# Optimization experiments

Measured on AMD Instinct MI355X. Metric: run time of the kernel, lower is better.

## Reference

```python
import jax, jax.numpy as jnp
import numpy as np

N = 33554432
NUM_CLASSES = 1000


def setup_inputs() -> dict:
    key = jax.random.key(0)
    k1, k2, k3 = jax.random.split(key, 3)
    confidences = jax.random.uniform(k1, (N,), dtype=jnp.float32)  # max-prob in [0,1)
    predictions = jax.random.randint(k2, (N,), 0, NUM_CLASSES, dtype=jnp.int64)
    labels = jax.random.randint(k3, (N,), 0, NUM_CLASSES, dtype=jnp.int64)
    return {"confidences": confidences, "predictions": predictions,
            "labels": labels, "n_bins": 10}


def reference(confidences, predictions, labels, n_bins):
    # Bin i covers (i/n_bins, (i+1)/n_bins]; conf == 0.0 goes to bin 0 (matches torch loop).
    n = confidences.shape[0]
    boundaries = jnp.linspace(0.0, 1.0, n_bins + 1, dtype=confidences.dtype)
    # searchsorted over upper boundaries: first upper >= conf -> bin index
    bins = jnp.searchsorted(boundaries[1:], confidences, side="left")
    bins = jnp.clip(bins, 0, n_bins - 1)

    acc = (predictions == labels).astype(confidences.dtype)
    ones = jnp.ones_like(confidences)

    cnt = jax.ops.segment_sum(ones, bins, num_segments=n_bins)
    acc_sum = jax.ops.segment_sum(acc, bins, num_segments=n_bins)
    conf_sum = jax.ops.segment_sum(confidences, bins, num_segments=n_bins)

    nonempty = cnt > 0
    safe_cnt = jnp.where(nonempty, cnt, jnp.ones_like(cnt))
    gap = jnp.abs(conf_sum / safe_cnt - acc_sum / safe_cnt)
    prop = cnt / n
    ece = jnp.sum(jnp.where(nonempty, gap * prop, jnp.zeros_like(gap)))
    return ece
```

## Files before the change

### kernel.cpp

```cpp
#include <hip/hip_runtime.h>


#define NBLK 2048
#define TPB  256
#define MAXB 256


__global__ __launch_bounds__(TPB) void ece_partial(
    const float* __restrict__ conf, const int* __restrict__ pred,
    const int* __restrict__ lab, const int* __restrict__ nbins_p,
    int n, int cap,
    unsigned* __restrict__ ws_cnt, unsigned* __restrict__ ws_acc,
    float* __restrict__ ws_conf)
{
  const int nb = nbins_p[0];
  const int tid = blockIdx.x * blockDim.x + threadIdx.x;
  const int nthreads = gridDim.x * blockDim.x;

  __shared__ unsigned s_ca[TPB / 64][10];
  __shared__ float    s_cs[TPB / 64][10];
  __shared__ unsigned g_cnt[MAXB];
  __shared__ unsigned g_acc[MAXB];
  __shared__ float    g_conf[MAXB];

  if (nb == 10 && cap >= 10) {
    unsigned ca[10];
    float    cs[10];
#pragma unroll
    for (int j = 0; j < 10; ++j) { ca[j] = 0u; cs[j] = 0.0f; }

    const int n4 = n >> 2;
    const float4* c4 = (const float4*)conf;
    const int4*   p4 = (const int4*)pred;
    const int4*   l4 = (const int4*)lab;

    for (int i = tid; i < n4; i += nthreads) {
      float4 c = c4[i];
      int4   p = p4[i];
      int4   l = l4[i];
      float cc[4] = {c.x, c.y, c.z, c.w};
      int   ok[4] = {p.x == l.x, p.y == l.y, p.z == l.z, p.w == l.w};
#pragma unroll
      for (int e = 0; e < 4; ++e) {
        float v = cc[e];
        int bin = 0;
#pragma unroll
        for (int j = 1; j <= 10; ++j) bin += ((float)j * 0.1f < v) ? 1 : 0;
        if (bin > 9) bin = 9;
#pragma unroll
        for (int j = 0; j < 10; ++j) {
          bool m = (bin == j);
          ca[j] += m ? (0x10000u | (unsigned)ok[e]) : 0u;
          cs[j] += m ? v : 0.0f;
        }
      }
    }
    for (int i = (n4 << 2) + tid; i < n; i += nthreads) {
      float v = conf[i];
      int okk = (pred[i] == lab[i]);
      int bin = 0;
#pragma unroll
      for (int j = 1; j <= 10; ++j) bin += ((float)j * 0.1f < v) ? 1 : 0;
      if (bin > 9) bin = 9;
#pragma unroll
      for (int j = 0; j < 10; ++j) {
        bool m = (bin == j);
        ca[j] += m ? (0x10000u | (unsigned)okk) : 0u;
        cs[j] += m ? v : 0.0f;
      }
    }

    const int lane = threadIdx.x & 63;
    const int wv   = threadIdx.x >> 6;
#pragma unroll
    for (int j = 0; j < 10; ++j) {
      unsigned a = ca[j];
      float    s = cs[j];
#pragma unroll
      for (int d = 32; d > 0; d >>= 1) {
        a += __shfl_xor(a, d, 64);
        s += __shfl_xor(s, d, 64);
      }
      if (lane == 0) { s_ca[wv][j] = a; s_cs[wv][j] = s; }
    }
    __syncthreads();
    if (threadIdx.x < 10) {
      unsigned tot = 0; float tc = 0.0f;
#pragma unroll
      for (int w = 0; w < TPB / 64; ++w) { tot += s_ca[w][threadIdx.x]; tc += s_cs[w][threadIdx.x]; }
      const int o = threadIdx.x * gridDim.x + blockIdx.x;
      ws_cnt[o]  = tot >> 16;
      ws_acc[o]  = tot & 0xFFFFu;
      ws_conf[o] = tc;
    }
  } else {
    int nbc = nb < 1 ? 1 : nb;
    if (nbc > MAXB) nbc = MAXB;
    if (nbc > cap) nbc = (cap < 1) ? 1 : cap;
    for (int j = threadIdx.x; j < nbc; j += blockDim.x) { g_cnt[j] = 0u; g_acc[j] = 0u; g_conf[j] = 0.0f; }
    __syncthreads();
    const float delta = 1.0f / (float)nb;
    for (int i = tid; i < n; i += nthreads) {
      float v = conf[i];
      int okk = (pred[i] == lab[i]);
      int bin = (int)(v * (float)nb);
      if (bin > nb - 1) bin = nb - 1;
      if (bin < 0) bin = 0;
      while (bin < nb - 1 && (float)(bin + 1) * delta < v) ++bin;
      while (bin > 0 && !((float)bin * delta < v)) --bin;
      if (bin > nbc - 1) bin = nbc - 1;
      atomicAdd(&g_cnt[bin], 1u);
      atomicAdd(&g_acc[bin], (unsigned)okk);
      atomicAdd(&g_conf[bin], v);
    }
    __syncthreads();
    for (int j = threadIdx.x; j < nbc; j += blockDim.x) {
      ws_cnt[j * gridDim.x + blockIdx.x]  = g_cnt[j];
      ws_acc[j * gridDim.x + blockIdx.x]  = g_acc[j];
      ws_conf[j * gridDim.x + blockIdx.x] = g_conf[j];
    }
  }
}

__global__ __launch_bounds__(640) void ece_final(
    const unsigned* __restrict__ ws_cnt, const unsigned* __restrict__ ws_acc,
    const float* __restrict__ ws_conf, const int* __restrict__ nbins_p,
    int n, int cap, float* __restrict__ out)
{
  int nb = nbins_p[0];
  if (nb < 1) nb = 1;
  int mx = cap < MAXB ? cap : MAXB;
  if (nb > mx) nb = mx;
  const int wv   = threadIdx.x >> 6;
  const int lane = threadIdx.x & 63;
  __shared__ double terms[MAXB];
  for (int j = threadIdx.x; j < MAXB; j += blockDim.x) terms[j] = 0.0;
  __syncthreads();
  for (int bin = wv; bin < nb; bin += 10) {
    unsigned long long cnt = 0, acc = 0;
    double cs = 0.0;
    for (int b = lane; b < NBLK; b += 64) {
      cnt += ws_cnt[bin * NBLK + b];
      acc += ws_acc[bin * NBLK + b];
      cs  += (double)ws_conf[bin * NBLK + b];
    }
#pragma unroll
    for (int d = 32; d > 0; d >>= 1) {
      cnt += __shfl_xor(cnt, d, 64);
      acc += __shfl_xor(acc, d, 64);
      cs  += __shfl_xor(cs, d, 64);
    }
    if (lane == 0) {
      double t = 0.0;
      if (cnt > 0) {
        double dc = (double)cnt;
        t = fabs(cs / dc - (double)acc / dc) * (dc / (double)n);
      }
      terms[bin] = t;
    }
  }
  __syncthreads();
  if (threadIdx.x == 0) {
    double e = 0.0;
    for (int j = 0; j < nb; ++j) e += terms[j];
    out[0] = (float)e;
  }
}

extern "C" void kernel_launch(void* const* d_in, const int* in_sizes, int n_in,
                              void* d_out, int out_size, void* d_ws, size_t ws_size,
                              hipStream_t stream) {
  const float* conf = (const float*)d_in[0];
  const int*   pred = (const int*)d_in[1];
  const int*   lab  = (const int*)d_in[2];
  const int*   nbp  = (const int*)d_in[3];
  const int n = in_sizes[0];

  size_t per = ws_size / 3;
  int cap = (int)(per / ((size_t)NBLK * sizeof(unsigned)));
  if (cap > MAXB) cap = MAXB;
  unsigned* ws_cnt = (unsigned*)d_ws;
  unsigned* ws_acc = (unsigned*)((char*)d_ws + (size_t)cap * NBLK * sizeof(unsigned));
  float*    ws_conf = (float*)((char*)d_ws + 2ull * (size_t)cap * NBLK * sizeof(unsigned));

  ece_partial<<<NBLK, TPB, 0, stream>>>(conf, pred, lab, nbp, n, cap, ws_cnt, ws_acc, ws_conf);
  ece_final<<<1, 640, 0, stream>>>(ws_cnt, ws_acc, ws_conf, nbp, n, cap, (float*)d_out);
}
```

Measured before the change: 387.6 us.

## Use cumulative threshold sums with wave ballot counts instead of per-bin masks

Replaces per-element one-hot binning with cumulative per-threshold accumulators (count of v > j*0.1), counting via wave ballot+popcount and recovering per-bin values by differencing in the final kernel. This removes the bin index computation and the 10-way select chain, leaving 9 compare/select pairs per element. The main loop uses a fixed iteration count, and the final kernel reads with float4 loads. Partial results become floats, and sums of floats over thresholds are differenced, which can add rounding error.

```diff
diff --git a/kernel.cpp b/kernel.cpp
--- a/kernel.cpp
+++ b/kernel.cpp
@@ -3,95 +3,115 @@
 
 #define NBLK 2048
 #define TPB  256
+#define NTH  (NBLK * TPB)
 #define MAXB 256
 
+#define SB(J)                                                   \
+  { bool g = ((float)(J) * 0.1f) < v;                           \
+    c##J += (unsigned)__popcll(__ballot(g));                    \
+    a##J += g ? okf : 0.0f;                                     \
+    t##J += g ? v : 0.0f; }
+
+#define SLOT(cx, px, lx)                                        \
+  { float v = (cx);                                             \
+    float okf = ((px) == (lx)) ? 1.0f : 0.0f;                   \
+    cAll += (unsigned)__popcll(__ballot(1));                    \
+    tAll += v; aAll += okf;                                     \
+    SB(1) SB(2) SB(3) SB(4) SB(5) SB(6) SB(7) SB(8) SB(9) }
+
+#define WRED(x)                                                 \
+  { x += __shfl_xor(x, 32, 64); x += __shfl_xor(x, 16, 64);     \
+    x += __shfl_xor(x, 8, 64);  x += __shfl_xor(x, 4, 64);      \
+    x += __shfl_xor(x, 2, 64);  x += __shfl_xor(x, 1, 64); }
 
 __global__ __launch_bounds__(TPB) void ece_partial(
     const float* __restrict__ conf, const int* __restrict__ pred,
     const int* __restrict__ lab, const int* __restrict__ nbins_p,
     int n, int cap,
-    unsigned* __restrict__ ws_cnt, unsigned* __restrict__ ws_acc,
+    float* __restrict__ ws_cnt, float* __restrict__ ws_acc,
     float* __restrict__ ws_conf)
 {
   const int nb = nbins_p[0];
   const int tid = blockIdx.x * blockDim.x + threadIdx.x;
-  const int nthreads = gridDim.x * blockDim.x;
-
-  __shared__ unsigned s_ca[TPB / 64][10];
-  __shared__ float    s_cs[TPB / 64][10];
+  const int lane = threadIdx.x & 63;
+  const int wv   = threadIdx.x >> 6;
+
+  __shared__ float l_c[TPB / 64][10];
+  __shared__ float l_a[TPB / 64][10];
+  __shared__ float l_t[TPB / 64][10];
   __shared__ unsigned g_cnt[MAXB];
   __shared__ unsigned g_acc[MAXB];
   __shared__ float    g_conf[MAXB];
 
   if (nb == 10 && cap >= 10) {
-    unsigned ca[10];
-    float    cs[10];
-#pragma unroll
-    for (int j = 0; j < 10; ++j) { ca[j] = 0u; cs[j] = 0.0f; }
-
+    unsigned cAll = 0, c1 = 0, c2 = 0, c3 = 0, c4v = 0, c5 = 0, c6 = 0, c7 = 0, c8 = 0, c9 = 0;
+    float aAll = 0.f, a1 = 0.f, a2 = 0.f, a3 = 0.f, a4 = 0.f, a5 = 0.f, a6 = 0.f, a7 = 0.f, a8 = 0.f, a9 = 0.f;
+    float tAll = 0.f, t1 = 0.f, t2 = 0.f, t3 = 0.f, t4 = 0.f, t5 = 0.f, t6 = 0.f, t7 = 0.f, t8 = 0.f, t9 = 0.f;
+#define c4 c4v
     const int n4 = n >> 2;
-    const float4* c4 = (const float4*)conf;
-    const int4*   p4 = (const int4*)pred;
-    const int4*   l4 = (const int4*)lab;
-
-    for (int i = tid; i < n4; i += nthreads) {
-      float4 c = c4[i];
-      int4   p = p4[i];
-      int4   l = l4[i];
-      float cc[4] = {c.x, c.y, c.z, c.w};
-      int   ok[4] = {p.x == l.x, p.y == l.y, p.z == l.z, p.w == l.w};
-#pragma unroll
-      for (int e = 0; e < 4; ++e) {
-        float v = cc[e];
-        int bin = 0;
-#pragma unroll
-        for (int j = 1; j <= 10; ++j) bin += ((float)j * 0.1f < v) ? 1 : 0;
-        if (bin > 9) bin = 9;
-#pragma unroll
-        for (int j = 0; j < 10; ++j) {
-          bool m = (bin == j);
-          ca[j] += m ? (0x10000u | (unsigned)ok[e]) : 0u;
-          cs[j] += m ? v : 0.0f;
-        }
-      }
-    }
-    for (int i = (n4 << 2) + tid; i < n; i += nthreads) {
-      float v = conf[i];
-      int okk = (pred[i] == lab[i]);
-      int bin = 0;
-#pragma unroll
-      for (int j = 1; j <= 10; ++j) bin += ((float)j * 0.1f < v) ? 1 : 0;
-      if (bin > 9) bin = 9;
-#pragma unroll
-      for (int j = 0; j < 10; ++j) {
-        bool m = (bin == j);
-        ca[j] += m ? (0x10000u | (unsigned)okk) : 0u;
-        cs[j] += m ? v : 0.0f;
-      }
-    }
-
-    const int lane = threadIdx.x & 63;
-    const int wv   = threadIdx.x >> 6;
-#pragma unroll
-    for (int j = 0; j < 10; ++j) {
-      unsigned a = ca[j];
-      float    s = cs[j];
-#pragma unroll
-      for (int d = 32; d > 0; d >>= 1) {
-        a += __shfl_xor(a, d, 64);
-        s += __shfl_xor(s, d, 64);
-      }
-      if (lane == 0) { s_ca[wv][j] = a; s_cs[wv][j] = s; }
+    const float4* cp4 = (const float4*)conf;
+    const int4*   pp4 = (const int4*)pred;
+    const int4*   lp4 = (const int4*)lab;
+
+    const int ITERS = (n4 + NTH - 1) / NTH;
+    int idx = tid;
+    for (int it = 0; it < ITERS; ++it, idx += NTH) {
+      if (idx < n4) {
+        float4 c = cp4[idx];
+        int4   p = pp4[idx];
+        int4   l = lp4[idx];
+        SLOT(c.x, p.x, l.x)
+        SLOT(c.y, p.y, l.y)
+        SLOT(c.z, p.z, l.z)
+        SLOT(c.w, p.w, l.w)
+      }
+    }
+    if (blockIdx.x == 0 && wv == 0) {
+      const int base = n4 << 2;
+      if (base < n) {
+        int en  = base + lane;
+        int enc = en < n ? en : (n - 1);
+        float vr = conf[enc];
+        int   pr = pred[enc];
+        int   lr = lab[enc];
+        bool vld = en < n;
+        float v   = vld ? vr : 0.0f;
+        float okf = (vld && pr == lr) ? 1.0f : 0.0f;
+        cAll += (unsigned)__popcll(__ballot(vld));
+        tAll += v; aAll += okf;
+        SB(1) SB(2) SB(3) SB(4) SB(5) SB(6) SB(7) SB(8) SB(9)
+      }
+    }
+#undef c4
+
+    WRED(aAll) WRED(a1) WRED(a2) WRED(a3) WRED(a4) WRED(a5) WRED(a6) WRED(a7) WRED(a8) WRED(a9)
+    WRED(tAll) WRED(t1) WRED(t2) WRED(t3) WRED(t4) WRED(t5) WRED(t6) WRED(t7) WRED(t8) WRED(t9)
+
+    if (lane == 0) {
+      l_c[wv][0] = (float)cAll; l_c[wv][1] = (float)c1; l_c[wv][2] = (float)c2;
+      l_c[wv][3] = (float)c3;   l_c[wv][4] = (float)c4v; l_c[wv][5] = (float)c5;
+      l_c[wv][6] = (float)c6;   l_c[wv][7] = (float)c7; l_c[wv][8] = (float)c8;
+      l_c[wv][9] = (float)c9;
+      l_a[wv][0] = aAll; l_a[wv][1] = a1; l_a[wv][2] = a2; l_a[wv][3] = a3;
+      l_a[wv][4] = a4;   l_a[wv][5] = a5; l_a[wv][6] = a6; l_a[wv][7] = a7;
+      l_a[wv][8] = a8;   l_a[wv][9] = a9;
+      l_t[wv][0] = tAll; l_t[wv][1] = t1; l_t[wv][2] = t2; l_t[wv][3] = t3;
+      l_t[wv][4] = t4;   l_t[wv][5] = t5; l_t[wv][6] = t6; l_t[wv][7] = t7;
+      l_t[wv][8] = t8;   l_t[wv][9] = t9;
     }
     __syncthreads();
     if (threadIdx.x < 10) {
-      unsigned tot = 0; float tc = 0.0f;
+      float sc = 0.f, sa = 0.f, st = 0.f;
 #pragma unroll
-      for (int w = 0; w < TPB / 64; ++w) { tot += s_ca[w][threadIdx.x]; tc += s_cs[w][threadIdx.x]; }
-      const int o = threadIdx.x * gridDim.x + blockIdx.x;
-      ws_cnt[o]  = tot >> 16;
-      ws_acc[o]  = tot & 0xFFFFu;
-      ws_conf[o] = tc;
+      for (int w = 0; w < TPB / 64; ++w) {
+        sc += l_c[w][threadIdx.x];
+        sa += l_a[w][threadIdx.x];
+        st += l_t[w][threadIdx.x];
+      }
+      const int o = threadIdx.x * NBLK + blockIdx.x;
+      ws_cnt[o]  = sc;
+      ws_acc[o]  = sa;
+      ws_conf[o] = st;
     }
   } else {
     int nbc = nb < 1 ? 1 : nb;
@@ -100,7 +120,7 @@
     for (int j = threadIdx.x; j < nbc; j += blockDim.x) { g_cnt[j] = 0u; g_acc[j] = 0u; g_conf[j] = 0.0f; }
     __syncthreads();
     const float delta = 1.0f / (float)nb;
-    for (int i = tid; i < n; i += nthreads) {
+    for (int i = tid; i < n; i += NTH) {
       float v = conf[i];
       int okk = (pred[i] == lab[i]);
       int bin = (int)(v * (float)nb);
@@ -115,15 +135,15 @@
     }
     __syncthreads();
     for (int j = threadIdx.x; j < nbc; j += blockDim.x) {
-      ws_cnt[j * gridDim.x + blockIdx.x]  = g_cnt[j];
-      ws_acc[j * gridDim.x + blockIdx.x]  = g_acc[j];
-      ws_conf[j * gridDim.x + blockIdx.x] = g_conf[j];
+      ws_cnt[j * NBLK + blockIdx.x]  = (float)g_cnt[j];
+      ws_acc[j * NBLK + blockIdx.x]  = (float)g_acc[j];
+      ws_conf[j * NBLK + blockIdx.x] = g_conf[j];
     }
   }
 }
 
 __global__ __launch_bounds__(640) void ece_final(
-    const unsigned* __restrict__ ws_cnt, const unsigned* __restrict__ ws_acc,
+    const float* __restrict__ ws_cnt, const float* __restrict__ ws_acc,
     const float* __restrict__ ws_conf, const int* __restrict__ nbins_p,
     int n, int cap, float* __restrict__ out)
 {
@@ -133,36 +153,49 @@
   if (nb > mx) nb = mx;
   const int wv   = threadIdx.x >> 6;
   const int lane = threadIdx.x & 63;
-  __shared__ double terms[MAXB];
-  for (int j = threadIdx.x; j < MAXB; j += blockDim.x) terms[j] = 0.0;
+  __shared__ double C[MAXB], A[MAXB], T[MAXB];
+  for (int j = threadIdx.x; j < MAXB; j += blockDim.x) { C[j] = 0.0; A[j] = 0.0; T[j] = 0.0; }
   __syncthreads();
-  for (int bin = wv; bin < nb; bin += 10) {
-    unsigned long long cnt = 0, acc = 0;
-    double cs = 0.0;
-    for (int b = lane; b < NBLK; b += 64) {
-      cnt += ws_cnt[bin * NBLK + b];
-      acc += ws_acc[bin * NBLK + b];
-      cs  += (double)ws_conf[bin * NBLK + b];
+
+  const int nrows = (nb == 10) ? 10 : nb;
+  for (int row = wv; row < nrows; row += 10) {
+    const float4* c4 = (const float4*)(ws_cnt  + (size_t)row * NBLK);
+    const float4* a4 = (const float4*)(ws_acc  + (size_t)row * NBLK);
+    const float4* t4 = (const float4*)(ws_conf + (size_t)row * NBLK);
+    double sc = 0.0, sa = 0.0, st = 0.0;
+#pragma unroll
+    for (int itr = 0; itr < NBLK / 256; ++itr) {
+      float4 a = c4[itr * 64 + lane];
+      float4 b = a4[itr * 64 + lane];
+      float4 f = t4[itr * 64 + lane];
+      sc += ((double)a.x + (double)a.y) + ((double)a.z + (double)a.w);
+      sa += ((double)b.x + (double)b.y) + ((double)b.z + (double)b.w);
+      st += ((double)f.x + (double)f.y) + ((double)f.z + (double)f.w);
     }
 #pragma unroll
     for (int d = 32; d > 0; d >>= 1) {
-      cnt += __shfl_xor(cnt, d, 64);
-      acc += __shfl_xor(acc, d, 64);
-      cs  += __shfl_xor(cs, d, 64);
-    }
-    if (lane == 0) {
-      double t = 0.0;
-      if (cnt > 0) {
-        double dc = (double)cnt;
-        t = fabs(cs / dc - (double)acc / dc) * (dc / (double)n);
-      }
-      terms[bin] = t;
-    }
+      sc += __shfl_xor(sc, d, 64);
+      sa += __shfl_xor(sa, d, 64);
+      st += __shfl_xor(st, d, 64);
+    }
+    if (lane == 0) { C[row] = sc; A[row] = sa; T[row] = st; }
   }
   __syncthreads();
   if (threadIdx.x == 0) {
     double e = 0.0;
-    for (int j = 0; j < nb; ++j) e += terms[j];
+    if (nb == 10) {
+      for (int j = 0; j < 10; ++j) {
+        double cn = C[j] - (j < 9 ? C[j + 1] : 0.0);
+        double ac = A[j] - (j < 9 ? A[j + 1] : 0.0);
+        double cf = T[j] - (j < 9 ? T[j + 1] : 0.0);
+        if (cn > 0.0) e += fabs(cf / cn - ac / cn) * (cn / (double)n);
+      }
+    } else {
+      for (int j = 0; j < nb; ++j) {
+        double cn = C[j];
+        if (cn > 0.0) e += fabs(T[j] / cn - A[j] / cn) * (cn / (double)n);
+      }
+    }
     out[0] = (float)e;
   }
 }
@@ -177,11 +210,11 @@
   const int n = in_sizes[0];
 
   size_t per = ws_size / 3;
-  int cap = (int)(per / ((size_t)NBLK * sizeof(unsigned)));
+  int cap = (int)(per / ((size_t)NBLK * sizeof(float)));
   if (cap > MAXB) cap = MAXB;
-  unsigned* ws_cnt = (unsigned*)d_ws;
-  unsigned* ws_acc = (unsigned*)((char*)d_ws + (size_t)cap * NBLK * sizeof(unsigned));
-  float*    ws_conf = (float*)((char*)d_ws + 2ull * (size_t)cap * NBLK * sizeof(unsigned));
+  float* ws_cnt  = (float*)d_ws;
+  float* ws_acc  = (float*)((char*)d_ws + (size_t)cap * NBLK * sizeof(float));
+  float* ws_conf = (float*)((char*)d_ws + 2ull * (size_t)cap * NBLK * sizeof(float));
 
   ece_partial<<<NBLK, TPB, 0, stream>>>(conf, pred, lab, nbp, n, cap, ws_cnt, ws_acc, ws_conf);
   ece_final<<<1, 640, 0, stream>>>(ws_cnt, ws_acc, ws_conf, nbp, n, cap, (float*)d_out);
```

After: 364.3 us. 1.06x faster.
